# Kernel optimization log

Measured on AMD Instinct MI355X. Metric: run time of the kernel, lower is better.

The kernel has to match this reference:

```python
import jax, jax.numpy as jnp
import numpy as np

BIG = 1e10  # large finite stand-in for +inf (avoids nan in logsumexp grads)
GAMMA = 1.0


def _dist_matrix(x, y):
    # squared euclidean pairwise distances: [B, N, M]
    x2 = jnp.sum(x * x, axis=-1)[:, :, None]
    y2 = jnp.sum(y * y, axis=-1)[:, None, :]
    xy = jnp.einsum('bnd,bmd->bnm', x, y)
    return x2 + y2 - 2.0 * xy


def _softdtw(D, gamma):
    # anti-diagonal wavefront soft-DTW DP via lax.scan
    B, N, M = D.shape
    i = jnp.arange(N + 1)                       # row index 0..N on each diagonal
    k = jnp.arange(2, N + M + 1)                # diagonal indices (i + j = k)
    j = k[:, None] - i[None, :]                 # [T, N+1] column index
    valid = (i[None, :] >= 1) & (j >= 1) & (j <= M)
    # skewed cost: Dskew[t, b, i] = D[b, i-1, k[t]-i-1] (garbage where invalid, masked out)
    r = jnp.clip(i - 1, 0, N - 1)               # [N+1]
    c = jnp.clip(j - 1, 0, M - 1)               # [T, N+1]
    Dskew = jnp.moveaxis(D[:, r[None, :], c], 1, 0)  # [T, B, N+1]

    d0 = jnp.full((B, N + 1), BIG, D.dtype).at[:, 0].set(0.0)  # diag k=0: R[0,0]=0
    d1 = jnp.full((B, N + 1), BIG, D.dtype)                     # diag k=1: all border inf

    pad = jnp.full((B, 1), BIG, D.dtype)

    def step(carry, xs):
        dm2, dm1 = carry
        dk, mask = xs
        r_diag = jnp.concatenate([pad, dm2[:, :-1]], axis=1)  # R[i-1, j-1]
        r_up = jnp.concatenate([pad, dm1[:, :-1]], axis=1)    # R[i-1, j]
        r_left = dm1                                          # R[i, j-1]
        softmin = -gamma * jax.scipy.special.logsumexp(
            jnp.stack([-r_diag, -r_up, -r_left], axis=0) / gamma, axis=0)
        new = jnp.where(mask[None, :], dk + softmin, BIG)
        return (dm1, new), None

    (_, last), _ = jax.lax.scan(step, (d0, d1), (Dskew, valid))
    return last[:, N]  # R[N, M] per batch element


def setup_inputs() -> dict:
    key = jax.random.key(0)
    kx, ky = jax.random.split(key)
    x = jax.random.normal(kx, (128, 256, 8), dtype=jnp.float32)
    y = jax.random.normal(ky, (128, 256, 8), dtype=jnp.float32)
    return {"x": x, "y": y}


def reference(x, y):
    D = _dist_matrix(x, y)
    return _softdtw(D, GAMMA)
```

## Files before the change

kernel.cpp:

```cpp
#include <hip/hip_runtime.h>

#ifndef __has_builtin
#define __has_builtin(x) 0
#endif

#if __has_builtin(__builtin_amdgcn_logf)
__device__ __forceinline__ float flog2(float x) { return __builtin_amdgcn_logf(x); }
#else
__device__ __forceinline__ float flog2(float x) { return log2f(x); }
#endif
#if __has_builtin(__builtin_amdgcn_exp2f)
__device__ __forceinline__ float fexp2(float x) { return __builtin_amdgcn_exp2f(x); }
#else
__device__ __forceinline__ float fexp2(float x) { return exp2f(x); }
#endif

#define L2E 1.4426950408889634f
#define LN2 0.6931471805599453
#define BIGL (1.0e10f * L2E)

template <int CTRL, int RM, int BM>
__device__ __forceinline__ float dpp_f(float v, float old) {
  int r = __builtin_amdgcn_update_dpp(__builtin_bit_cast(int, old),
                                      __builtin_bit_cast(int, v),
                                      CTRL, RM, BM, false);
  return __builtin_bit_cast(float, r);
}

__device__ __forceinline__ double shup1z_d(double v) {
  int lo = __double2loint(v), hi = __double2hiint(v);
  int lo2 = __builtin_amdgcn_update_dpp(0, lo, 0x138, 0xF, 0xF, false);
  int hi2 = __builtin_amdgcn_update_dpp(0, hi, 0x138, 0xF, 0xF, false);
  return __hiloint2double(hi2, lo2);
}

__device__ __forceinline__ float wave_max63(float m) {
  m = fmaxf(m, dpp_f<0x111, 0xF, 0xF>(m, m));
  m = fmaxf(m, dpp_f<0x112, 0xF, 0xF>(m, m));
  m = fmaxf(m, dpp_f<0x114, 0xF, 0xF>(m, m));
  m = fmaxf(m, dpp_f<0x118, 0xF, 0xF>(m, m));
  m = fmaxf(m, dpp_f<0x142, 0xA, 0xF>(m, m));
  m = fmaxf(m, dpp_f<0x143, 0xC, 0xF>(m, m));
  return m;
}

__global__ __launch_bounds__(256) void softdtw_prep(
    const float* __restrict__ x, const float* __restrict__ y,
    uint2* __restrict__ Kpack, int B)
{
  const int b  = blockIdx.x % B;
  const int K0 = (blockIdx.x / B) << 6;
  const int i0 = threadIdx.x;

  __shared__ __align__(8) unsigned short tileK[64][256];

  const float* xb = x + ((size_t)b * 256 + i0) * 8;
  float4 xa = *(const float4*)(xb);
  float4 xc = *(const float4*)(xb + 4);
  const float* yb = y + (size_t)b * 256 * 8;

  for (int jj = 0; jj < 64; ++jj) {
    int j0 = K0 + jj - i0;
    bool valid = (unsigned)j0 < 256u;
    int jc = j0 < 0 ? 0 : (j0 > 255 ? 255 : j0);
    const float4* yp = (const float4*)(yb + jc * 8);
    float4 ya = yp[0], yc = yp[1];
    float d, D;
    d = xa.x - ya.x; D = d * d;
    d = xa.y - ya.y; D = fmaf(d, d, D);
    d = xa.z - ya.z; D = fmaf(d, d, D);
    d = xa.w - ya.w; D = fmaf(d, d, D);
    d = xc.x - yc.x; D = fmaf(d, d, D);
    d = xc.y - yc.y; D = fmaf(d, d, D);
    d = xc.z - yc.z; D = fmaf(d, d, D);
    d = xc.w - yc.w; D = fmaf(d, d, D);
    float K = valid ? fexp2(-L2E * D) : 0.0f;
    unsigned kb = __builtin_bit_cast(unsigned, K);
    unsigned rn = (kb + 0x7FFFu + ((kb >> 16) & 1u)) >> 16;
    tileK[jj][i0] = (unsigned short)rn;
  }
  __syncthreads();

  const size_t obase = (size_t)b * 511 * 64;
  #pragma unroll
  for (int w = 0; w < 16; ++w) {
    int p = threadIdx.x + (w << 8);
    int kkL = p >> 6, tt = p & 63;
    int kk = K0 + kkL;
    if (kk < 511) {
      uint2 v = *(const uint2*)&tileK[kkL][tt * 4];
      Kpack[obase + (size_t)kk * 64 + tt] = v;
    }
  }
}

__global__ __launch_bounds__(64) void softdtw_dp(
    const uint2* __restrict__ Kpack, float* __restrict__ out)
{
  const int b = blockIdx.x;
  const int t = threadIdx.x;

  const char* kptr = (const char*)(Kpack + (size_t)b * 511 * 64) + t * 8;

  uint2 kr[8];
  #pragma unroll
  for (int q = 0; q < 8; ++q) kr[q] = *(const uint2*)(kptr + q * 512);

  double EA[4] = {0.0, 0.0, 0.0, 0.0};
  double EB[4] = {0.0, 0.0, 0.0, 0.0};
  double dgc = 0.0;
  int Csum = 0;

#define DPSTEP(q, E2, E1, FIRST, PF) do {                                     \
    uint2 kb_ = kr[q];                                                        \
    if (PF) kr[q] = *(const uint2*)(kptr + (q) * 512);                        \
    double K0_ = (double)__builtin_bit_cast(float, kb_.x << 16);              \
    double K1_ = (double)__builtin_bit_cast(float, kb_.x & 0xFFFF0000u);      \
    double K2_ = (double)__builtin_bit_cast(float, kb_.y << 16);              \
    double K3_ = (double)__builtin_bit_cast(float, kb_.y & 0xFFFF0000u);      \
    double up_ = shup1z_d(E1[3]);                                             \
    double dg_ = dgc;                                                         \
    if (FIRST) dg_ = (t == 0) ? 1.0 : dg_;                                    \
    double V0_ = K0_ * (dg_   + (up_   + E1[0]));                             \
    double V1_ = K1_ * (E2[0] + (E1[0] + E1[1]));                             \
    double V2_ = K2_ * (E2[1] + (E1[1] + E1[2]));                             \
    double V3_ = K3_ * (E2[2] + (E1[2] + E1[3]));                             \
    dgc = up_;                                                                \
    E2[0] = V0_; E2[1] = V1_; E2[2] = V2_; E2[3] = V3_;                       \
  } while (0)

#define RENORM(EN, EO) do {                                                   \
    double m4_ = fmax(fmax(EN[0], EN[1]), fmax(EN[2], EN[3]));                \
    float mh_ = __builtin_bit_cast(float, __double2hiint(m4_));               \
    mh_ = wave_max63(mh_);                                                    \
    int mb_ = __builtin_amdgcn_readlane(__builtin_bit_cast(int, mh_), 63);    \
    int s_ = (mb_ == 0) ? 0 : (1873 - ((mb_ >> 20) & 0x7FF));                 \
    EN[0] = ldexp(EN[0], s_); EN[1] = ldexp(EN[1], s_);                       \
    EN[2] = ldexp(EN[2], s_); EN[3] = ldexp(EN[3], s_);                       \
    EO[0] = ldexp(EO[0], s_); EO[1] = ldexp(EO[1], s_);                       \
    EO[2] = ldexp(EO[2], s_); EO[3] = ldexp(EO[3], s_);                       \
    dgc = ldexp(dgc, s_);                                                     \
    Csum += s_;                                                               \
  } while (0)

  kptr += 4096;
  DPSTEP(0, EA, EB, true,  true);
  DPSTEP(1, EB, EA, false, true);
  DPSTEP(2, EA, EB, false, true);
  DPSTEP(3, EB, EA, false, true);
  DPSTEP(4, EA, EB, false, true);
  DPSTEP(5, EB, EA, false, true);
  DPSTEP(6, EA, EB, false, true);
  DPSTEP(7, EB, EA, false, true);
  RENORM(EB, EA);
  for (int blk = 1; blk < 63; ++blk) {
    kptr += 4096;
    DPSTEP(0, EA, EB, false, true);
    DPSTEP(1, EB, EA, false, true);
    DPSTEP(2, EA, EB, false, true);
    DPSTEP(3, EB, EA, false, true);
    DPSTEP(4, EA, EB, false, true);
    DPSTEP(5, EB, EA, false, true);
    DPSTEP(6, EA, EB, false, true);
    DPSTEP(7, EB, EA, false, true);
    RENORM(EB, EA);
  }
  DPSTEP(0, EA, EB, false, false);
  DPSTEP(1, EB, EA, false, false);
  DPSTEP(2, EA, EB, false, false);
  DPSTEP(3, EB, EA, false, false);
  DPSTEP(4, EA, EB, false, false);
  DPSTEP(5, EB, EA, false, false);
  DPSTEP(6, EA, EB, false, false);

  if (t == 63) {
    int ex;
    double mant = frexp(EA[3], &ex);
    float l2 = (float)ex + flog2((float)mant);
    out[b] = (float)(LN2 * ((double)Csum - (double)l2));
  }
}

__global__ __launch_bounds__(64) void softdtw_fallback(
    const float* __restrict__ x, const float* __restrict__ y,
    float* __restrict__ out)
{
  const int b = blockIdx.x;
  const int t = threadIdx.x;
  __shared__ float zbuf[4][64][9];
  const float* xb = x + (size_t)b * 256 * 8;
  const float* yb = y + (size_t)b * 256 * 8;
  float xe[4][9];
  float x2L[4];
  #pragma unroll
  for (int r = 0; r < 4; ++r) {
    const int row = 4 * t + r;
    float4 a = *(const float4*)(yb + row * 8);
    float4 c = *(const float4*)(yb + row * 8 + 4);
    float y2 = a.x*a.x + a.y*a.y + a.z*a.z + a.w*a.w
             + c.x*c.x + c.y*c.y + c.z*c.z + c.w*c.w;
    float* zr = &zbuf[r][t][0];
    zr[0] = -2.0f*L2E*a.x; zr[1] = -2.0f*L2E*a.y; zr[2] = -2.0f*L2E*a.z; zr[3] = -2.0f*L2E*a.w;
    zr[4] = -2.0f*L2E*c.x; zr[5] = -2.0f*L2E*c.y; zr[6] = -2.0f*L2E*c.z; zr[7] = -2.0f*L2E*c.w;
    zr[8] = L2E * y2;
    float4 xa = *(const float4*)(xb + row * 8);
    float4 xc = *(const float4*)(xb + row * 8 + 4);
    xe[r][0]=xa.x; xe[r][1]=xa.y; xe[r][2]=xa.z; xe[r][3]=xa.w;
    xe[r][4]=xc.x; xe[r][5]=xc.y; xe[r][6]=xc.z; xe[r][7]=xc.w; xe[r][8]=1.0f;
    x2L[r] = L2E*(xa.x*xa.x + xa.y*xa.y + xa.z*xa.z + xa.w*xa.w
                + xc.x*xc.x + xc.y*xc.y + xc.z*xc.z + xc.w*xc.w);
  }
  __syncthreads();
  float zA[9], zB[9], zC[9], zD[9];
  #pragma unroll
  for (int w = 0; w < 9; ++w) { zA[w]=0.f; zB[w]=0.f; zC[w]=0.f; zD[w]=0.f; }
  float RA[4] = {BIGL,BIGL,BIGL,BIGL};
  float RB[4] = {BIGL,BIGL,BIGL,BIGL};
  int u = -4 * t;
  auto ROW = [&](int r, float a, float bb, float c, const float (&zr)[9]) -> float {
    float acc = x2L[r];
    #pragma unroll
    for (int d = 0; d < 9; ++d) acc = fmaf(xe[r][d], zr[d], acc);
    float m = fminf(fminf(a, bb), c);
    float e = fexp2(m-a) + fexp2(m-bb) + fexp2(m-c);
    float val = acc + (m - flog2(e));
    return ((unsigned)(u - r) < 256u) ? val : BIGL;
  };
  auto STEP = [&](float (&zw)[9], const float (&zx)[9], const float (&zy)[9],
                  const float (&zz)[9], float (&Rm2)[4], float (&Rm1)[4],
                  int p, int k) {
    int uc = u < 0 ? 0 : (u > 255 ? 255 : u);
    const float* zp = &zbuf[p][uc >> 2][0];
    #pragma unroll
    for (int w = 0; w < 9; ++w) zw[w] = zp[w];
    float up_in = __shfl_up(Rm1[3], 1);
    float dg_in = __shfl_up(Rm2[3], 1);
    float bval = (k == 2) ? 0.0f : BIGL;
    if (t == 0) { up_in = BIGL; dg_in = bval; }
    float n0 = ROW(0, dg_in,  up_in,  Rm1[0], zw);
    float n1 = ROW(1, Rm2[0], Rm1[0], Rm1[1], zx);
    float n2 = ROW(2, Rm2[1], Rm1[1], Rm1[2], zy);
    float n3 = ROW(3, Rm2[2], Rm1[2], Rm1[3], zz);
    Rm2[0]=n0; Rm2[1]=n1; Rm2[2]=n2; Rm2[3]=n3;
    u += 1;
  };
  int k = 2;
  for (int mi = 0; mi < 127; ++mi) {
    STEP(zD, zA, zB, zC, RA, RB, 0, k);
    STEP(zC, zD, zA, zB, RB, RA, 1, k + 1);
    STEP(zB, zC, zD, zA, RA, RB, 2, k + 2);
    STEP(zA, zB, zC, zD, RB, RA, 3, k + 3);
    k += 4;
  }
  STEP(zD, zA, zB, zC, RA, RB, 0, k);
  STEP(zC, zD, zA, zB, RB, RA, 1, k + 1);
  STEP(zB, zC, zD, zA, RA, RB, 2, k + 2);
  if (t == 63) out[b] = RA[3] * LN2;
}

extern "C" void kernel_launch(void* const* d_in, const int* in_sizes, int n_in,
                              void* d_out, int out_size, void* d_ws, size_t ws_size,
                              hipStream_t stream) {
  const float* x = (const float*)d_in[0];
  const float* y = (const float*)d_in[1];
  float* out = (float*)d_out;
  const int B = in_sizes[0] / (256 * 8);
  const size_t need = (size_t)B * 511 * 64 * 8 + 512;
  if (ws_size >= need) {
    uint2* Kpack = (uint2*)d_ws;
    softdtw_prep<<<dim3(B * 8), dim3(256), 0, stream>>>(x, y, Kpack, B);
    softdtw_dp<<<dim3(B), dim3(64), 0, stream>>>(Kpack, out);
  } else {
    softdtw_fallback<<<dim3(B), dim3(64), 0, stream>>>(x, y, out);
  }
}
```

Measured before the change: 61.64 us.

## Pack two diagonals per 16-byte load and double-buffer K prefetch in DP

The prep kernel now writes pairs of consecutive anti-diagonals as one uint4 per lane, padded to 512 diagonals so the bounds check goes away. The DP kernel issues eight 16-byte loads per 16-diagonal chunk into one register buffer while computing from the other, with a sched_barrier to keep the loads ahead of the math. Renormalisation now runs every 8 steps with a smaller target exponent, likely to give headroom for the changed schedule. This uses more registers and a larger workspace in return for fewer, wider loads and a longer prefetch distance on the serial dependency chain.

```diff
diff --git a/kernel.cpp b/kernel.cpp
--- a/kernel.cpp
+++ b/kernel.cpp
@@ -46,13 +46,13 @@
 
 __global__ __launch_bounds__(256) void softdtw_prep(
     const float* __restrict__ x, const float* __restrict__ y,
-    uint2* __restrict__ Kpack, int B)
+    uint4* __restrict__ Kp4, int B)
 {
   const int b  = blockIdx.x % B;
   const int K0 = (blockIdx.x / B) << 6;
   const int i0 = threadIdx.x;
 
-  __shared__ __align__(8) unsigned short tileK[64][256];
+  __shared__ __align__(16) unsigned short tileK[64][256];
 
   const float* xb = x + ((size_t)b * 256 + i0) * 8;
   float4 xa = *(const float4*)(xb);
@@ -81,46 +81,40 @@
   }
   __syncthreads();
 
-  const size_t obase = (size_t)b * 511 * 64;
+  const size_t obase4 = (size_t)b * 16384;
   #pragma unroll
-  for (int w = 0; w < 16; ++w) {
+  for (int w = 0; w < 8; ++w) {
     int p = threadIdx.x + (w << 8);
-    int kkL = p >> 6, tt = p & 63;
-    int kk = K0 + kkL;
-    if (kk < 511) {
-      uint2 v = *(const uint2*)&tileK[kkL][tt * 4];
-      Kpack[obase + (size_t)kk * 64 + tt] = v;
-    }
+    int kkP = p >> 6;
+    int tt = p & 63;
+    uint2 lo = *(const uint2*)&tileK[kkP * 2][tt * 4];
+    uint2 hi = *(const uint2*)&tileK[kkP * 2 + 1][tt * 4];
+    uint4 v; v.x = lo.x; v.y = lo.y; v.z = hi.x; v.w = hi.y;
+    Kp4[obase4 + (size_t)((K0 >> 1) + kkP) * 64 + tt] = v;
   }
 }
 
 __global__ __launch_bounds__(64) void softdtw_dp(
-    const uint2* __restrict__ Kpack, float* __restrict__ out)
+    const uint4* __restrict__ Kp4, float* __restrict__ out)
 {
   const int b = blockIdx.x;
   const int t = threadIdx.x;
 
-  const char* kptr = (const char*)(Kpack + (size_t)b * 511 * 64) + t * 8;
-
-  uint2 kr[8];
-  #pragma unroll
-  for (int q = 0; q < 8; ++q) kr[q] = *(const uint2*)(kptr + q * 512);
+  const char* kbase = (const char*)(Kp4 + (size_t)b * 16384) + t * 16;
 
   double EA[4] = {0.0, 0.0, 0.0, 0.0};
   double EB[4] = {0.0, 0.0, 0.0, 0.0};
   double dgc = 0.0;
   int Csum = 0;
 
-#define DPSTEP(q, E2, E1, FIRST, PF) do {                                     \
-    uint2 kb_ = kr[q];                                                        \
-    if (PF) kr[q] = *(const uint2*)(kptr + (q) * 512);                        \
-    double K0_ = (double)__builtin_bit_cast(float, kb_.x << 16);              \
-    double K1_ = (double)__builtin_bit_cast(float, kb_.x & 0xFFFF0000u);      \
-    double K2_ = (double)__builtin_bit_cast(float, kb_.y << 16);              \
-    double K3_ = (double)__builtin_bit_cast(float, kb_.y & 0xFFFF0000u);      \
+#define DPSTEP2(KAw, KBw, E2, E1, FIRSTF) do {                                \
+    double K0_ = (double)__builtin_bit_cast(float, (KAw) << 16);              \
+    double K1_ = (double)__builtin_bit_cast(float, (KAw) & 0xFFFF0000u);      \
+    double K2_ = (double)__builtin_bit_cast(float, (KBw) << 16);              \
+    double K3_ = (double)__builtin_bit_cast(float, (KBw) & 0xFFFF0000u);      \
     double up_ = shup1z_d(E1[3]);                                             \
     double dg_ = dgc;                                                         \
-    if (FIRST) dg_ = (t == 0) ? 1.0 : dg_;                                    \
+    if (FIRSTF) dg_ = (t == 0) ? 1.0 : dg_;                                   \
     double V0_ = K0_ * (dg_   + (up_   + E1[0]));                             \
     double V1_ = K1_ * (E2[0] + (E1[0] + E1[1]));                             \
     double V2_ = K2_ * (E2[1] + (E1[1] + E1[2]));                             \
@@ -134,7 +128,7 @@
     float mh_ = __builtin_bit_cast(float, __double2hiint(m4_));               \
     mh_ = wave_max63(mh_);                                                    \
     int mb_ = __builtin_amdgcn_readlane(__builtin_bit_cast(int, mh_), 63);    \
-    int s_ = (mb_ == 0) ? 0 : (1873 - ((mb_ >> 20) & 0x7FF));                 \
+    int s_ = (mb_ == 0) ? 0 : (1823 - ((mb_ >> 20) & 0x7FF));                 \
     EN[0] = ldexp(EN[0], s_); EN[1] = ldexp(EN[1], s_);                       \
     EN[2] = ldexp(EN[2], s_); EN[3] = ldexp(EN[3], s_);                       \
     EO[0] = ldexp(EO[0], s_); EO[1] = ldexp(EO[1], s_);                       \
@@ -143,35 +137,70 @@
     Csum += s_;                                                               \
   } while (0)
 
-  kptr += 4096;
-  DPSTEP(0, EA, EB, true,  true);
-  DPSTEP(1, EB, EA, false, true);
-  DPSTEP(2, EA, EB, false, true);
-  DPSTEP(3, EB, EA, false, true);
-  DPSTEP(4, EA, EB, false, true);
-  DPSTEP(5, EB, EA, false, true);
-  DPSTEP(6, EA, EB, false, true);
-  DPSTEP(7, EB, EA, false, true);
+#define CHUNK16(CB, LB, FIRSTF) do {                                          \
+    LB[0] = *(const uint4*)(kbase);                                           \
+    LB[1] = *(const uint4*)(kbase + 1024);                                    \
+    LB[2] = *(const uint4*)(kbase + 2048);                                    \
+    LB[3] = *(const uint4*)(kbase + 3072);                                    \
+    LB[4] = *(const uint4*)(kbase + 4096);                                    \
+    LB[5] = *(const uint4*)(kbase + 5120);                                    \
+    LB[6] = *(const uint4*)(kbase + 6144);                                    \
+    LB[7] = *(const uint4*)(kbase + 7168);                                    \
+    kbase += 8192;                                                            \
+    __builtin_amdgcn_sched_barrier(0);                                        \
+    DPSTEP2(CB[0].x, CB[0].y, EA, EB, FIRSTF);                                \
+    DPSTEP2(CB[0].z, CB[0].w, EB, EA, false);                                 \
+    DPSTEP2(CB[1].x, CB[1].y, EA, EB, false);                                 \
+    DPSTEP2(CB[1].z, CB[1].w, EB, EA, false);                                 \
+    DPSTEP2(CB[2].x, CB[2].y, EA, EB, false);                                 \
+    DPSTEP2(CB[2].z, CB[2].w, EB, EA, false);                                 \
+    DPSTEP2(CB[3].x, CB[3].y, EA, EB, false);                                 \
+    DPSTEP2(CB[3].z, CB[3].w, EB, EA, false);                                 \
+    RENORM(EB, EA);                                                           \
+    DPSTEP2(CB[4].x, CB[4].y, EA, EB, false);                                 \
+    DPSTEP2(CB[4].z, CB[4].w, EB, EA, false);                                 \
+    DPSTEP2(CB[5].x, CB[5].y, EA, EB, false);                                 \
+    DPSTEP2(CB[5].z, CB[5].w, EB, EA, false);                                 \
+    DPSTEP2(CB[6].x, CB[6].y, EA, EB, false);                                 \
+    DPSTEP2(CB[6].z, CB[6].w, EB, EA, false);                                 \
+    DPSTEP2(CB[7].x, CB[7].y, EA, EB, false);                                 \
+    DPSTEP2(CB[7].z, CB[7].w, EB, EA, false);                                 \
+    RENORM(EB, EA);                                                           \
+  } while (0)
+
+  uint4 KA[8], KB[8];
+  KA[0] = *(const uint4*)(kbase);
+  KA[1] = *(const uint4*)(kbase + 1024);
+  KA[2] = *(const uint4*)(kbase + 2048);
+  KA[3] = *(const uint4*)(kbase + 3072);
+  KA[4] = *(const uint4*)(kbase + 4096);
+  KA[5] = *(const uint4*)(kbase + 5120);
+  KA[6] = *(const uint4*)(kbase + 6144);
+  KA[7] = *(const uint4*)(kbase + 7168);
+  kbase += 8192;
+
+  CHUNK16(KA, KB, true);
+  #pragma unroll 1
+  for (int c = 0; c < 15; ++c) {
+    CHUNK16(KB, KA, false);
+    CHUNK16(KA, KB, false);
+  }
+  DPSTEP2(KB[0].x, KB[0].y, EA, EB, false);
+  DPSTEP2(KB[0].z, KB[0].w, EB, EA, false);
+  DPSTEP2(KB[1].x, KB[1].y, EA, EB, false);
+  DPSTEP2(KB[1].z, KB[1].w, EB, EA, false);
+  DPSTEP2(KB[2].x, KB[2].y, EA, EB, false);
+  DPSTEP2(KB[2].z, KB[2].w, EB, EA, false);
+  DPSTEP2(KB[3].x, KB[3].y, EA, EB, false);
+  DPSTEP2(KB[3].z, KB[3].w, EB, EA, false);
   RENORM(EB, EA);
-  for (int blk = 1; blk < 63; ++blk) {
-    kptr += 4096;
-    DPSTEP(0, EA, EB, false, true);
-    DPSTEP(1, EB, EA, false, true);
-    DPSTEP(2, EA, EB, false, true);
-    DPSTEP(3, EB, EA, false, true);
-    DPSTEP(4, EA, EB, false, true);
-    DPSTEP(5, EB, EA, false, true);
-    DPSTEP(6, EA, EB, false, true);
-    DPSTEP(7, EB, EA, false, true);
-    RENORM(EB, EA);
-  }
-  DPSTEP(0, EA, EB, false, false);
-  DPSTEP(1, EB, EA, false, false);
-  DPSTEP(2, EA, EB, false, false);
-  DPSTEP(3, EB, EA, false, false);
-  DPSTEP(4, EA, EB, false, false);
-  DPSTEP(5, EB, EA, false, false);
-  DPSTEP(6, EA, EB, false, false);
+  DPSTEP2(KB[4].x, KB[4].y, EA, EB, false);
+  DPSTEP2(KB[4].z, KB[4].w, EB, EA, false);
+  DPSTEP2(KB[5].x, KB[5].y, EA, EB, false);
+  DPSTEP2(KB[5].z, KB[5].w, EB, EA, false);
+  DPSTEP2(KB[6].x, KB[6].y, EA, EB, false);
+  DPSTEP2(KB[6].z, KB[6].w, EB, EA, false);
+  DPSTEP2(KB[7].x, KB[7].y, EA, EB, false);
 
   if (t == 63) {
     int ex;
@@ -265,11 +294,11 @@
   const float* y = (const float*)d_in[1];
   float* out = (float*)d_out;
   const int B = in_sizes[0] / (256 * 8);
-  const size_t need = (size_t)B * 511 * 64 * 8 + 512;
+  const size_t need = (size_t)B * 262144;
   if (ws_size >= need) {
-    uint2* Kpack = (uint2*)d_ws;
-    softdtw_prep<<<dim3(B * 8), dim3(256), 0, stream>>>(x, y, Kpack, B);
-    softdtw_dp<<<dim3(B), dim3(64), 0, stream>>>(Kpack, out);
+    uint4* Kp4 = (uint4*)d_ws;
+    softdtw_prep<<<dim3(B * 8), dim3(256), 0, stream>>>(x, y, Kp4, B);
+    softdtw_dp<<<dim3(B), dim3(64), 0, stream>>>(Kp4, out);
   } else {
     softdtw_fallback<<<dim3(B), dim3(64), 0, stream>>>(x, y, out);
   }
```

Result: faster. 55.84 us (-9.4%).

## Split DP rows into two skewed halves per lane to shorten the serial dependency chain

Applied to the files above, without the earlier changes.

Each lane now owns two rows in the top half and two rows in the bottom half, instead of four consecutive rows. The bottom half runs three diagonals behind the top half, and a lane-rotated FIFO hands the boundary values from top to bottom. The goal is two independent, shorter dependency chains per step, which gives more instruction-level parallelism in the serial wavefront. The prep kernel writes a new uint4 layout with four diagonals per 16-byte load to match, and the renorm exponent offset is lowered. The cost is added complexity, more registers for the FIFO and for renorming it, and some risk to numerical headroom.

```diff
diff --git a/kernel.cpp b/kernel.cpp
--- a/kernel.cpp
+++ b/kernel.cpp
@@ -34,6 +34,13 @@
   return __hiloint2double(hi2, lo2);
 }
 
+__device__ __forceinline__ double ror1_d(double v) {
+  int lo = __double2loint(v), hi = __double2hiint(v);
+  int lo2 = __builtin_amdgcn_update_dpp(0, lo, 0x13C, 0xF, 0xF, false);
+  int hi2 = __builtin_amdgcn_update_dpp(0, hi, 0x13C, 0xF, 0xF, false);
+  return __hiloint2double(hi2, lo2);
+}
+
 __device__ __forceinline__ float wave_max63(float m) {
   m = fmaxf(m, dpp_f<0x111, 0xF, 0xF>(m, m));
   m = fmaxf(m, dpp_f<0x112, 0xF, 0xF>(m, m));
@@ -46,13 +53,13 @@
 
 __global__ __launch_bounds__(256) void softdtw_prep(
     const float* __restrict__ x, const float* __restrict__ y,
-    uint2* __restrict__ Kpack, int B)
+    uint4* __restrict__ Kp4, int B)
 {
   const int b  = blockIdx.x % B;
   const int K0 = (blockIdx.x / B) << 6;
   const int i0 = threadIdx.x;
 
-  __shared__ __align__(8) unsigned short tileK[64][256];
+  __shared__ __align__(16) unsigned short tileK[64][256];
 
   const float* xb = x + ((size_t)b * 256 + i0) * 8;
   float4 xa = *(const float4*)(xb);
@@ -81,101 +88,129 @@
   }
   __syncthreads();
 
-  const size_t obase = (size_t)b * 511 * 64;
+  const size_t obase4 = (size_t)b * 16384;
   #pragma unroll
-  for (int w = 0; w < 16; ++w) {
+  for (int w = 0; w < 8; ++w) {
     int p = threadIdx.x + (w << 8);
-    int kkL = p >> 6, tt = p & 63;
-    int kk = K0 + kkL;
-    if (kk < 511) {
-      uint2 v = *(const uint2*)&tileK[kkL][tt * 4];
-      Kpack[obase + (size_t)kk * 64 + tt] = v;
-    }
+    int c  = p >> 10;
+    int qL = (p >> 6) & 15;
+    int tt = p & 63;
+    int kkL = qL * 4;
+    uint4 v;
+    v.x = *(const unsigned*)&tileK[kkL + 0][128 * c + 2 * tt];
+    v.y = *(const unsigned*)&tileK[kkL + 1][128 * c + 2 * tt];
+    v.z = *(const unsigned*)&tileK[kkL + 2][128 * c + 2 * tt];
+    v.w = *(const unsigned*)&tileK[kkL + 3][128 * c + 2 * tt];
+    Kp4[obase4 + (size_t)c * 8192 + (size_t)((K0 >> 2) + qL) * 64 + tt] = v;
   }
 }
 
 __global__ __launch_bounds__(64) void softdtw_dp(
-    const uint2* __restrict__ Kpack, float* __restrict__ out)
+    const uint4* __restrict__ Kp4, float* __restrict__ out)
 {
   const int b = blockIdx.x;
   const int t = threadIdx.x;
 
-  const char* kptr = (const char*)(Kpack + (size_t)b * 511 * 64) + t * 8;
-
-  uint2 kr[8];
-  #pragma unroll
-  for (int q = 0; q < 8; ++q) kr[q] = *(const uint2*)(kptr + q * 512);
-
-  double EA[4] = {0.0, 0.0, 0.0, 0.0};
-  double EB[4] = {0.0, 0.0, 0.0, 0.0};
-  double dgc = 0.0;
+  const char* pA = (const char*)(Kp4 + (size_t)b * 16384) + t * 16;
+  const char* pB = pA + 131072;
+
+  double EA_A[2] = {0.0, 0.0}, EB_A[2] = {0.0, 0.0};
+  double EA_B[2] = {0.0, 0.0}, EB_B[2] = {0.0, 0.0};
+  double fifo[8] = {0.0, 0.0, 0.0, 0.0, 0.0, 0.0, 0.0, 0.0};
+  double dgcA = 0.0, dgcB = 0.0;
   int Csum = 0;
 
-#define DPSTEP(q, E2, E1, FIRST, PF) do {                                     \
-    uint2 kb_ = kr[q];                                                        \
-    if (PF) kr[q] = *(const uint2*)(kptr + (q) * 512);                        \
-    double K0_ = (double)__builtin_bit_cast(float, kb_.x << 16);              \
-    double K1_ = (double)__builtin_bit_cast(float, kb_.x & 0xFFFF0000u);      \
-    double K2_ = (double)__builtin_bit_cast(float, kb_.y << 16);              \
-    double K3_ = (double)__builtin_bit_cast(float, kb_.y & 0xFFFF0000u);      \
-    double up_ = shup1z_d(E1[3]);                                             \
-    double dg_ = dgc;                                                         \
-    if (FIRST) dg_ = (t == 0) ? 1.0 : dg_;                                    \
-    double V0_ = K0_ * (dg_   + (up_   + E1[0]));                             \
-    double V1_ = K1_ * (E2[0] + (E1[0] + E1[1]));                             \
-    double V2_ = K2_ * (E2[1] + (E1[1] + E1[2]));                             \
-    double V3_ = K3_ * (E2[2] + (E1[2] + E1[3]));                             \
-    dgc = up_;                                                                \
-    E2[0] = V0_; E2[1] = V1_; E2[2] = V2_; E2[3] = V3_;                       \
+#define STEPAB(sr, wA, wB, NA, PA, NB, PB, FIRSTF) do {                       \
+    double KA0_ = (double)__builtin_bit_cast(float, (unsigned)(wA) << 16);    \
+    double KA1_ = (double)__builtin_bit_cast(float, (unsigned)(wA) & 0xFFFF0000u); \
+    double KB0_ = (double)__builtin_bit_cast(float, (unsigned)(wB) << 16);    \
+    double KB1_ = (double)__builtin_bit_cast(float, (unsigned)(wB) & 0xFFFF0000u); \
+    double upA_ = shup1z_d(PA[1]);                                            \
+    double dgA_ = dgcA;                                                       \
+    if (FIRSTF) dgA_ = (t == 0) ? 1.0 : dgA_;                                 \
+    double nA0_ = KA0_ * (dgA_ + (upA_ + PA[0]));                             \
+    double nA1_ = KA1_ * (NA[0] + (PA[0] + PA[1]));                           \
+    dgcA = upA_; NA[0] = nA0_; NA[1] = nA1_;                                  \
+    fifo[(sr) & 7] = ror1_d(nA1_);                                            \
+    double upBr_ = shup1z_d(PB[1]);                                           \
+    double upB_ = (t == 0) ? fifo[((sr) + 3) & 7] : upBr_;                    \
+    double nB0_ = KB0_ * (dgcB + (upB_ + PB[0]));                             \
+    double nB1_ = KB1_ * (NB[0] + (PB[0] + PB[1]));                           \
+    dgcB = upB_; NB[0] = nB0_; NB[1] = nB1_;                                  \
   } while (0)
 
-#define RENORM(EN, EO) do {                                                   \
-    double m4_ = fmax(fmax(EN[0], EN[1]), fmax(EN[2], EN[3]));                \
+#define RENORM2() do {                                                        \
+    double m4_ = fmax(fmax(EB_A[0], EB_A[1]), fmax(EB_B[0], EB_B[1]));        \
     float mh_ = __builtin_bit_cast(float, __double2hiint(m4_));               \
     mh_ = wave_max63(mh_);                                                    \
     int mb_ = __builtin_amdgcn_readlane(__builtin_bit_cast(int, mh_), 63);    \
-    int s_ = (mb_ == 0) ? 0 : (1873 - ((mb_ >> 20) & 0x7FF));                 \
-    EN[0] = ldexp(EN[0], s_); EN[1] = ldexp(EN[1], s_);                       \
-    EN[2] = ldexp(EN[2], s_); EN[3] = ldexp(EN[3], s_);                       \
-    EO[0] = ldexp(EO[0], s_); EO[1] = ldexp(EO[1], s_);                       \
-    EO[2] = ldexp(EO[2], s_); EO[3] = ldexp(EO[3], s_);                       \
-    dgc = ldexp(dgc, s_);                                                     \
+    int s_ = (mb_ == 0) ? 0 : (1823 - ((mb_ >> 20) & 0x7FF));                 \
+    EB_A[0] = ldexp(EB_A[0], s_); EB_A[1] = ldexp(EB_A[1], s_);               \
+    EA_A[0] = ldexp(EA_A[0], s_); EA_A[1] = ldexp(EA_A[1], s_);               \
+    EB_B[0] = ldexp(EB_B[0], s_); EB_B[1] = ldexp(EB_B[1], s_);               \
+    EA_B[0] = ldexp(EA_B[0], s_); EA_B[1] = ldexp(EA_B[1], s_);               \
+    dgcA = ldexp(dgcA, s_); dgcB = ldexp(dgcB, s_);                           \
+    fifo[0] = ldexp(fifo[0], s_); fifo[1] = ldexp(fifo[1], s_);               \
+    fifo[2] = ldexp(fifo[2], s_); fifo[3] = ldexp(fifo[3], s_);               \
+    fifo[4] = ldexp(fifo[4], s_); fifo[5] = ldexp(fifo[5], s_);               \
+    fifo[6] = ldexp(fifo[6], s_); fifo[7] = ldexp(fifo[7], s_);               \
     Csum += s_;                                                               \
   } while (0)
 
-  kptr += 4096;
-  DPSTEP(0, EA, EB, true,  true);
-  DPSTEP(1, EB, EA, false, true);
-  DPSTEP(2, EA, EB, false, true);
-  DPSTEP(3, EB, EA, false, true);
-  DPSTEP(4, EA, EB, false, true);
-  DPSTEP(5, EB, EA, false, true);
-  DPSTEP(6, EA, EB, false, true);
-  DPSTEP(7, EB, EA, false, true);
-  RENORM(EB, EA);
-  for (int blk = 1; blk < 63; ++blk) {
-    kptr += 4096;
-    DPSTEP(0, EA, EB, false, true);
-    DPSTEP(1, EB, EA, false, true);
-    DPSTEP(2, EA, EB, false, true);
-    DPSTEP(3, EB, EA, false, true);
-    DPSTEP(4, EA, EB, false, true);
-    DPSTEP(5, EB, EA, false, true);
-    DPSTEP(6, EA, EB, false, true);
-    DPSTEP(7, EB, EA, false, true);
-    RENORM(EB, EA);
-  }
-  DPSTEP(0, EA, EB, false, false);
-  DPSTEP(1, EB, EA, false, false);
-  DPSTEP(2, EA, EB, false, false);
-  DPSTEP(3, EB, EA, false, false);
-  DPSTEP(4, EA, EB, false, false);
-  DPSTEP(5, EB, EA, false, false);
-  DPSTEP(6, EA, EB, false, false);
+#define BODY8(A0_, A1_, B0_, B1_, LA0_, LA1_, LB0_, LB1_, FIRSTF, PF) do {    \
+    if (PF) {                                                                 \
+      LA0_ = *(const uint4*)(pA);                                             \
+      LA1_ = *(const uint4*)(pA + 1024);                                      \
+      LB0_ = *(const uint4*)(pB);                                             \
+      LB1_ = *(const uint4*)(pB + 1024);                                      \
+      pA += 2048; pB += 2048;                                                 \
+    }                                                                         \
+    __builtin_amdgcn_sched_barrier(0);                                        \
+    STEPAB(0, (A0_).x, (B0_).x, EA_A, EB_A, EA_B, EB_B, FIRSTF);              \
+    STEPAB(1, (A0_).y, (B0_).y, EB_A, EA_A, EB_B, EA_B, false);               \
+    STEPAB(2, (A0_).z, (B0_).z, EA_A, EB_A, EA_B, EB_B, false);               \
+    STEPAB(3, (A0_).w, (B0_).w, EB_A, EA_A, EB_B, EA_B, false);               \
+    STEPAB(4, (A1_).x, (B1_).x, EA_A, EB_A, EA_B, EB_B, false);               \
+    STEPAB(5, (A1_).y, (B1_).y, EB_A, EA_A, EB_B, EA_B, false);               \
+    STEPAB(6, (A1_).z, (B1_).z, EA_A, EB_A, EA_B, EB_B, false);               \
+    STEPAB(7, (A1_).w, (B1_).w, EB_A, EA_A, EB_B, EA_B, false);               \
+    RENORM2();                                                                \
+  } while (0)
+
+#define STEPBONLY(sr, wB, NB, PB) do {                                        \
+    double KB0_ = (double)__builtin_bit_cast(float, (unsigned)(wB) << 16);    \
+    double KB1_ = (double)__builtin_bit_cast(float, (unsigned)(wB) & 0xFFFF0000u); \
+    double upBr_ = shup1z_d(PB[1]);                                           \
+    double upB_ = (t == 0) ? fifo[((sr) + 3) & 7] : upBr_;                    \
+    double nB0_ = KB0_ * (dgcB + (upB_ + PB[0]));                             \
+    double nB1_ = KB1_ * (NB[0] + (PB[0] + PB[1]));                           \
+    dgcB = upB_; NB[0] = nB0_; NB[1] = nB1_;                                  \
+  } while (0)
+
+  uint4 AU0, AU1, BU0, BU1, AV0, AV1, BV0, BV1;
+  AU0 = *(const uint4*)(pA);
+  AU1 = *(const uint4*)(pA + 1024);
+  pA += 2048;
+  BU0.x = 0u; BU0.y = 0u; BU0.z = 0u; BU0.w = 0u;
+  BU1 = *(const uint4*)(pB);
+  pB += 1024;
+
+  BODY8(AU0, AU1, BU0, BU1, AV0, AV1, BV0, BV1, true, true);
+  #pragma unroll 1
+  for (int i = 0; i < 31; ++i) {
+    BODY8(AV0, AV1, BV0, BV1, AU0, AU1, BU0, BU1, false, true);
+    BODY8(AU0, AU1, BU0, BU1, AV0, AV1, BV0, BV1, false, true);
+  }
+  uint4 BT = *(const uint4*)(pB);
+  BODY8(AV0, AV1, BV0, BV1, AU0, AU1, BU0, BU1, false, false);
+
+  STEPBONLY(0, BT.x, EA_B, EB_B);
+  STEPBONLY(1, BT.y, EB_B, EA_B);
+  STEPBONLY(2, BT.z, EA_B, EB_B);
 
   if (t == 63) {
     int ex;
-    double mant = frexp(EA[3], &ex);
+    double mant = frexp(EA_B[1], &ex);
     float l2 = (float)ex + flog2((float)mant);
     out[b] = (float)(LN2 * ((double)Csum - (double)l2));
   }
@@ -265,11 +300,11 @@
   const float* y = (const float*)d_in[1];
   float* out = (float*)d_out;
   const int B = in_sizes[0] / (256 * 8);
-  const size_t need = (size_t)B * 511 * 64 * 8 + 512;
+  const size_t need = (size_t)B * 262144;
   if (ws_size >= need) {
-    uint2* Kpack = (uint2*)d_ws;
-    softdtw_prep<<<dim3(B * 8), dim3(256), 0, stream>>>(x, y, Kpack, B);
-    softdtw_dp<<<dim3(B), dim3(64), 0, stream>>>(Kpack, out);
+    uint4* Kp4 = (uint4*)d_ws;
+    softdtw_prep<<<dim3(B * 8), dim3(256), 0, stream>>>(x, y, Kp4, B);
+    softdtw_dp<<<dim3(B), dim3(64), 0, stream>>>(Kp4, out);
   } else {
     softdtw_fallback<<<dim3(B), dim3(64), 0, stream>>>(x, y, out);
   }
```

Measured after the change: 65.20 us. 5.8% more time.
